# Performance work log

Measured on AMD Instinct MI355X. Metric: run time of the kernel, lower is better.

Reference implementation:

```python
import jax, jax.numpy as jnp
import numpy as np

N_NODES = 100000
N_EDGES = 1600000
D_IN = 64


def _graph_conv(x, edge_src, edge_dst, W, b, n_nodes):
    # gather source features along edges, mean-aggregate at destinations,
    # then linear transform + ReLU (standard GraphConv semantics)
    msgs = x[edge_src]  # [E, d]
    agg = jax.ops.segment_sum(msgs, edge_dst, num_segments=n_nodes)  # [N, d]
    deg = jax.ops.segment_sum(jnp.ones((edge_src.shape[0],), x.dtype), edge_dst,
                              num_segments=n_nodes)  # [N]
    agg = agg / jnp.maximum(deg, 1.0)[:, None]
    return jax.nn.relu(agg @ W + b)


def setup_inputs() -> dict:
    key = jax.random.key(0)
    ks = jax.random.split(key, 6)
    node_features = jax.random.normal(ks[0], (N_NODES, D_IN), dtype=jnp.float32)
    edge_src = jax.random.randint(ks[1], (N_EDGES,), 0, N_NODES)
    edge_dst = jax.random.randint(ks[2], (N_EDGES,), 0, N_NODES)
    W1 = jax.random.normal(ks[3], (D_IN, 64), dtype=jnp.float32) * (1.0 / np.sqrt(D_IN))
    b1 = jnp.zeros((64,), jnp.float32)
    W2 = jax.random.normal(ks[4], (64, 32), dtype=jnp.float32) * (1.0 / np.sqrt(64))
    b2 = jnp.zeros((32,), jnp.float32)
    Wd = jax.random.normal(ks[5], (1, 1), dtype=jnp.float32)
    bd = jnp.zeros((1,), jnp.float32)
    return {"node_features": node_features, "edge_src": edge_src, "edge_dst": edge_dst,
            "W1": W1, "b1": b1, "W2": W2, "b2": b2, "Wd": Wd, "bd": bd}


def reference(node_features, edge_src, edge_dst, W1, b1, W2, b2, Wd, bd):
    n_nodes = node_features.shape[0]
    x = _graph_conv(node_features, edge_src, edge_dst, W1, b1, n_nodes)  # [N, 64]
    x = _graph_conv(x, edge_src, edge_dst, W2, b2, n_nodes)              # [N, 32]
    x = jnp.mean(x, axis=1, keepdims=True)                               # [N, 1]
    return jax.nn.sigmoid(x @ Wd + bd)                                   # [N, 1]
```

## Files before the change

kernel.cpp:

```cpp
#include <hip/hip_runtime.h>
#include <hip/hip_bf16.h>

#define N_NODES 100000
#define N_EDGES 1600000
#define N_PAD   100096
#define BSHIFT  10
#define NBUCKET 98
#define BCAP    19456
#define EPB     4096
#define NSCAT   391
#define NGEMM1  1563
#define PCAP    34816
#define ZROW    N_NODES

__device__ __forceinline__ unsigned short f32_to_bf16(float f) {
    unsigned int u = __float_as_uint(f);
    unsigned int r = (u + 0x7fffu + ((u >> 16) & 1u)) >> 16;
    return (unsigned short)r;
}
__device__ __forceinline__ float bf16_lo(unsigned int p) {
    return __uint_as_float(p << 16);
}
__device__ __forceinline__ float bf16_hi(unsigned int p) {
    return __uint_as_float(p & 0xffff0000u);
}

__global__ void __launch_bounds__(256) k1_scatter_gemm64(
    const int* __restrict__ src, const int* __restrict__ dst,
    int* __restrict__ bcur, unsigned int* __restrict__ tmp,
    const float4* __restrict__ X4, const float* __restrict__ W,
    unsigned short* __restrict__ Y, int n_edges, int M) {
    extern __shared__ char smem[];
    int t = threadIdx.x;
    if (blockIdx.x < NSCAT) {
        int* lh = (int*)smem;
        int e0 = blockIdx.x * EPB;
        int e1 = min(e0 + EPB, n_edges);
        if (t < 128) lh[t] = 0;
        __syncthreads();
        int ls[16], ld[16];
        #pragma unroll
        for (int j = 0; j < 16; j++) {
            int e = e0 + t + j * 256;
            if (e < e1) {
                ls[j] = src[e];
                ld[j] = dst[e];
                atomicAdd(&lh[ld[j] >> BSHIFT], 1);
            }
        }
        __syncthreads();
        if (t < NBUCKET) {
            int c = lh[t];
            lh[t] = (c > 0) ? atomicAdd(&bcur[t], c) : 0;
        }
        __syncthreads();
        #pragma unroll
        for (int j = 0; j < 16; j++) {
            int e = e0 + t + j * 256;
            if (e < e1) {
                int b = ld[j] >> BSHIFT;
                int p = atomicAdd(&lh[b], 1);
                if (p < BCAP)
                    tmp[(size_t)b * BCAP + p] =
                        ((unsigned)ls[j] << BSHIFT) | (unsigned)(ld[j] & 1023);
            }
        }
        return;
    }
    float* sx = (float*)smem;
    float* sw = sx + 64 * 65;
    int base = (blockIdx.x - NSCAT) * 64;
    for (int i = t; i < 64 * 16; i += 256) {
        int r = i >> 4, c4 = i & 15;
        int row = base + r;
        float4 v = make_float4(0.f, 0.f, 0.f, 0.f);
        if (row < M) v = X4[(size_t)row * 16 + c4];
        sx[r * 65 + c4 * 4 + 0] = v.x; sx[r * 65 + c4 * 4 + 1] = v.y;
        sx[r * 65 + c4 * 4 + 2] = v.z; sx[r * 65 + c4 * 4 + 3] = v.w;
    }
    float4* sw4 = (float4*)sw;
    const float4* W4 = (const float4*)W;
    for (int i = t; i < 64 * 16; i += 256) sw4[i] = W4[i];
    __syncthreads();

    int tm = t & 15;
    int tn = t >> 4;
    float acc[4][4] = {{0.f}};
    #pragma unroll 8
    for (int k = 0; k < 64; k++) {
        float4 b = sw4[k * 16 + tn];
        float a0 = sx[(tm * 4 + 0) * 65 + k], a1 = sx[(tm * 4 + 1) * 65 + k];
        float a2 = sx[(tm * 4 + 2) * 65 + k], a3 = sx[(tm * 4 + 3) * 65 + k];
        acc[0][0] = fmaf(a0, b.x, acc[0][0]); acc[0][1] = fmaf(a0, b.y, acc[0][1]);
        acc[0][2] = fmaf(a0, b.z, acc[0][2]); acc[0][3] = fmaf(a0, b.w, acc[0][3]);
        acc[1][0] = fmaf(a1, b.x, acc[1][0]); acc[1][1] = fmaf(a1, b.y, acc[1][1]);
        acc[1][2] = fmaf(a1, b.z, acc[1][2]); acc[1][3] = fmaf(a1, b.w, acc[1][3]);
        acc[2][0] = fmaf(a2, b.x, acc[2][0]); acc[2][1] = fmaf(a2, b.y, acc[2][1]);
        acc[2][2] = fmaf(a2, b.z, acc[2][2]); acc[2][3] = fmaf(a2, b.w, acc[2][3]);
        acc[3][0] = fmaf(a3, b.x, acc[3][0]); acc[3][1] = fmaf(a3, b.y, acc[3][1]);
        acc[3][2] = fmaf(a3, b.z, acc[3][2]); acc[3][3] = fmaf(a3, b.w, acc[3][3]);
    }
    #pragma unroll
    for (int i = 0; i < 4; i++) {
        int row = base + tm * 4 + i;
        if (row <= M) {
            ushort4 p;
            p.x = f32_to_bf16(acc[i][0]); p.y = f32_to_bf16(acc[i][1]);
            p.z = f32_to_bf16(acc[i][2]); p.w = f32_to_bf16(acc[i][3]);
            *(ushort4*)&Y[(size_t)row * 64 + tn * 4] = p;
        }
    }
}

__global__ void __launch_bounds__(1024) bucket_to_csr(
    const unsigned int* __restrict__ tmp, const int* __restrict__ bcur,
    int2* __restrict__ meta, int* __restrict__ col, int n_nodes) {
    __shared__ int nh[1024];
    __shared__ int npref[1024];
    int b = blockIdx.x;
    int t = threadIdx.x;
    int m = min(bcur[b], BCAP);
    int cbase = b * PCAP;
    nh[t] = 0;
    __syncthreads();
    const unsigned int* te = tmp + (size_t)b * BCAP;
    for (int i = t; i < m; i += 1024) atomicAdd(&nh[te[i] & 1023], 1);
    __syncthreads();
    int d  = nh[t];
    int pc = (d + 31) & ~31;
    npref[t] = pc;
    __syncthreads();
    for (int off = 1; off < 1024; off <<= 1) {
        int u = (t >= off) ? npref[t - off] : 0;
        __syncthreads();
        npref[t] += u;
        __syncthreads();
    }
    int begin = cbase + npref[t] - pc;
    int node = (b << BSHIFT) + t;
    if (node < n_nodes) meta[node] = make_int2(begin, d);
    for (int j = d; j < pc; j++) col[begin + j] = ZROW;
    nh[t] = begin;
    __syncthreads();
    for (int i = t; i < m; i += 1024) {
        unsigned int e = te[i];
        int pos = atomicAdd(&nh[e & 1023], 1);
        col[pos] = (int)(e >> BSHIFT);
    }
}

__global__ void __launch_bounds__(256) gemm_n32(const float4* __restrict__ X4,
                                                const float* __restrict__ W,
                                                unsigned short* __restrict__ Z, int M) {
    __shared__ float sx[128][65];
    __shared__ float sw[64 * 32];
    int t = threadIdx.x;
    int base = blockIdx.x * 128;
    for (int i = t; i < 128 * 16; i += 256) {
        int r = i >> 4, c4 = i & 15;
        int row = base + r;
        float4 v = make_float4(0.f, 0.f, 0.f, 0.f);
        if (row < M) v = X4[(size_t)row * 16 + c4];
        sx[r][c4 * 4 + 0] = v.x; sx[r][c4 * 4 + 1] = v.y;
        sx[r][c4 * 4 + 2] = v.z; sx[r][c4 * 4 + 3] = v.w;
    }
    float4* sw4 = (float4*)sw;
    const float4* W4 = (const float4*)W;
    for (int i = t; i < 64 * 8; i += 256) sw4[i] = W4[i];
    __syncthreads();

    int tm = t & 31;
    int tn = t >> 5;
    float acc[4][4] = {{0.f}};
    #pragma unroll 8
    for (int k = 0; k < 64; k++) {
        float4 b = sw4[k * 8 + tn];
        float a0 = sx[tm * 4 + 0][k], a1 = sx[tm * 4 + 1][k];
        float a2 = sx[tm * 4 + 2][k], a3 = sx[tm * 4 + 3][k];
        acc[0][0] = fmaf(a0, b.x, acc[0][0]); acc[0][1] = fmaf(a0, b.y, acc[0][1]);
        acc[0][2] = fmaf(a0, b.z, acc[0][2]); acc[0][3] = fmaf(a0, b.w, acc[0][3]);
        acc[1][0] = fmaf(a1, b.x, acc[1][0]); acc[1][1] = fmaf(a1, b.y, acc[1][1]);
        acc[1][2] = fmaf(a1, b.z, acc[1][2]); acc[1][3] = fmaf(a1, b.w, acc[1][3]);
        acc[2][0] = fmaf(a2, b.x, acc[2][0]); acc[2][1] = fmaf(a2, b.y, acc[2][1]);
        acc[2][2] = fmaf(a2, b.z, acc[2][2]); acc[2][3] = fmaf(a2, b.w, acc[2][3]);
        acc[3][0] = fmaf(a3, b.x, acc[3][0]); acc[3][1] = fmaf(a3, b.y, acc[3][1]);
        acc[3][2] = fmaf(a3, b.z, acc[3][2]); acc[3][3] = fmaf(a3, b.w, acc[3][3]);
    }
    #pragma unroll
    for (int i = 0; i < 4; i++) {
        int row = base + tm * 4 + i;
        if (row <= M) {
            ushort4 p;
            p.x = f32_to_bf16(acc[i][0]); p.y = f32_to_bf16(acc[i][1]);
            p.z = f32_to_bf16(acc[i][2]); p.w = f32_to_bf16(acc[i][3]);
            *(ushort4*)&Z[(size_t)row * 32 + tn * 4] = p;
        }
    }
}

__global__ void __launch_bounds__(256) gather_relu64(
    const uint4* __restrict__ Y4, const int2* __restrict__ meta,
    const int* __restrict__ col, const float* __restrict__ b1,
    float4* __restrict__ H4, int n_nodes) {
    int n = blockIdx.x * 4 + (threadIdx.x >> 6);
    if (n >= n_nodes) return;
    int lane = threadIdx.x & 63;
    int g = lane >> 3;
    int c = lane & 7;
    int2 md = meta[n];
    int beg = md.x;
    int d = md.y;

    float acc[8] = {0.f, 0.f, 0.f, 0.f, 0.f, 0.f, 0.f, 0.f};
    for (int i = 0; i < d; i += 32) {
        int s0 = col[beg + i + g];
        int s1 = col[beg + i + g + 8];
        int s2 = col[beg + i + g + 16];
        int s3 = col[beg + i + g + 24];
        uint4 v0 = Y4[(size_t)s0 * 8 + c];
        uint4 v1 = Y4[(size_t)s1 * 8 + c];
        uint4 v2 = Y4[(size_t)s2 * 8 + c];
        uint4 v3 = Y4[(size_t)s3 * 8 + c];
        acc[0] += (bf16_lo(v0.x) + bf16_lo(v1.x)) + (bf16_lo(v2.x) + bf16_lo(v3.x));
        acc[1] += (bf16_hi(v0.x) + bf16_hi(v1.x)) + (bf16_hi(v2.x) + bf16_hi(v3.x));
        acc[2] += (bf16_lo(v0.y) + bf16_lo(v1.y)) + (bf16_lo(v2.y) + bf16_lo(v3.y));
        acc[3] += (bf16_hi(v0.y) + bf16_hi(v1.y)) + (bf16_hi(v2.y) + bf16_hi(v3.y));
        acc[4] += (bf16_lo(v0.z) + bf16_lo(v1.z)) + (bf16_lo(v2.z) + bf16_lo(v3.z));
        acc[5] += (bf16_hi(v0.z) + bf16_hi(v1.z)) + (bf16_hi(v2.z) + bf16_hi(v3.z));
        acc[6] += (bf16_lo(v0.w) + bf16_lo(v1.w)) + (bf16_lo(v2.w) + bf16_lo(v3.w));
        acc[7] += (bf16_hi(v0.w) + bf16_hi(v1.w)) + (bf16_hi(v2.w) + bf16_hi(v3.w));
    }
    #pragma unroll
    for (int m = 8; m <= 32; m <<= 1) {
        #pragma unroll
        for (int q = 0; q < 8; q++) acc[q] += __shfl_xor(acc[q], m);
    }
    float inv = 1.0f / fmaxf((float)d, 1.0f);
    const float4* b1_4 = (const float4*)b1;
    float4 ba = b1_4[c * 2], bb = b1_4[c * 2 + 1];
    if (g == 0) {
        float4 o0, o1;
        o0.x = fmaxf(fmaf(acc[0], inv, ba.x), 0.f);
        o0.y = fmaxf(fmaf(acc[1], inv, ba.y), 0.f);
        o0.z = fmaxf(fmaf(acc[2], inv, ba.z), 0.f);
        o0.w = fmaxf(fmaf(acc[3], inv, ba.w), 0.f);
        o1.x = fmaxf(fmaf(acc[4], inv, bb.x), 0.f);
        o1.y = fmaxf(fmaf(acc[5], inv, bb.y), 0.f);
        o1.z = fmaxf(fmaf(acc[6], inv, bb.z), 0.f);
        o1.w = fmaxf(fmaf(acc[7], inv, bb.w), 0.f);
        H4[(size_t)n * 16 + c * 2]     = o0;
        H4[(size_t)n * 16 + c * 2 + 1] = o1;
    }
}

__global__ void __launch_bounds__(256) gather_final32(
    const uint4* __restrict__ Z4, const int2* __restrict__ meta,
    const int* __restrict__ col, const float* __restrict__ b2,
    const float* __restrict__ Wd, const float* __restrict__ bd,
    float* __restrict__ out, int n_nodes) {
    int n = blockIdx.x * 4 + (threadIdx.x >> 6);
    if (n >= n_nodes) return;
    int lane = threadIdx.x & 63;
    int g = lane >> 2;
    int c = lane & 3;
    int2 md = meta[n];
    int beg = md.x;
    int d = md.y;

    float acc[8] = {0.f, 0.f, 0.f, 0.f, 0.f, 0.f, 0.f, 0.f};
    for (int i = 0; i < d; i += 32) {
        int s0 = col[beg + i + g];
        int s1 = col[beg + i + g + 16];
        uint4 v0 = Z4[(size_t)s0 * 4 + c];
        uint4 v1 = Z4[(size_t)s1 * 4 + c];
        acc[0] += bf16_lo(v0.x) + bf16_lo(v1.x);
        acc[1] += bf16_hi(v0.x) + bf16_hi(v1.x);
        acc[2] += bf16_lo(v0.y) + bf16_lo(v1.y);
        acc[3] += bf16_hi(v0.y) + bf16_hi(v1.y);
        acc[4] += bf16_lo(v0.z) + bf16_lo(v1.z);
        acc[5] += bf16_hi(v0.z) + bf16_hi(v1.z);
        acc[6] += bf16_lo(v0.w) + bf16_lo(v1.w);
        acc[7] += bf16_hi(v0.w) + bf16_hi(v1.w);
    }
    #pragma unroll
    for (int m = 4; m <= 32; m <<= 1) {
        #pragma unroll
        for (int q = 0; q < 8; q++) acc[q] += __shfl_xor(acc[q], m);
    }
    float inv = 1.0f / fmaxf((float)d, 1.0f);
    const float4* b2_4 = (const float4*)b2;
    float4 ba = b2_4[c * 2], bb = b2_4[c * 2 + 1];
    float local = 0.f;
    local += fmaxf(fmaf(acc[0], inv, ba.x), 0.f);
    local += fmaxf(fmaf(acc[1], inv, ba.y), 0.f);
    local += fmaxf(fmaf(acc[2], inv, ba.z), 0.f);
    local += fmaxf(fmaf(acc[3], inv, ba.w), 0.f);
    local += fmaxf(fmaf(acc[4], inv, bb.x), 0.f);
    local += fmaxf(fmaf(acc[5], inv, bb.y), 0.f);
    local += fmaxf(fmaf(acc[6], inv, bb.z), 0.f);
    local += fmaxf(fmaf(acc[7], inv, bb.w), 0.f);
    local += __shfl_xor(local, 1);
    local += __shfl_xor(local, 2);
    if (lane == 0) {
        float z = fmaf(local * (1.0f / 32.0f), Wd[0], bd[0]);
        out[n] = 1.0f / (1.0f + __expf(-z));
    }
}

extern "C" void kernel_launch(void* const* d_in, const int* in_sizes, int n_in,
                              void* d_out, int out_size, void* d_ws, size_t ws_size,
                              hipStream_t stream) {
    const float* x    = (const float*)d_in[0];
    const int*   esrc = (const int*)d_in[1];
    const int*   edst = (const int*)d_in[2];
    const float* W1   = (const float*)d_in[3];
    const float* b1   = (const float*)d_in[4];
    const float* W2   = (const float*)d_in[5];
    const float* b2   = (const float*)d_in[6];
    const float* Wd   = (const float*)d_in[7];
    const float* bd   = (const float*)d_in[8];
    float* out = (float*)d_out;

    int*  bcur = (int*)d_ws;
    int2* meta = (int2*)(bcur + 128);
    int*  col  = (int*)(meta + N_PAD);
    float* h   = (float*)(col + (size_t)NBUCKET * PCAP + 1024);
    unsigned int* tmp = (unsigned int*)h;
    unsigned short* y  = (unsigned short*)(h + (size_t)N_NODES * 64);
    unsigned short* z2 = y + (size_t)(N_NODES + 1) * 64;

    hipMemsetAsync((void*)bcur, 0, 128 * sizeof(int), stream);

    k1_scatter_gemm64<<<NSCAT + NGEMM1, 256, 33024, stream>>>(
        esrc, edst, bcur, tmp, (const float4*)x, W1, y, N_EDGES, N_NODES);
    bucket_to_csr<<<NBUCKET, 1024, 0, stream>>>(tmp, bcur, meta, col, N_NODES);
    gather_relu64<<<(N_NODES + 3) / 4, 256, 0, stream>>>(
        (const uint4*)y, meta, col, b1, (float4*)h, N_NODES);
    gemm_n32<<<(N_NODES + 127) / 128, 256, 0, stream>>>((const float4*)h, W2, z2, N_NODES);
    gather_final32<<<(N_NODES + 3) / 4, 256, 0, stream>>>(
        (const uint4*)z2, meta, col, b2, Wd, bd, out, N_NODES);
}
```

Baseline: 237.5 us.

## Fuse second-layer GEMM into first gather epilogue, widen final gather parallelism

The separate gemm_n32 kernel is removed. Each wave now multiplies its aggregated, ReLU'd 64-wide node row by W2 held in registers, reduces across lanes with shuffles and writes the bf16 result directly, so the fp32 intermediate h is never written to or read back from global memory. The final gather is remapped to 8 edge groups by 8 lanes with uint2 loads and four edges per iteration, to keep more loads in flight. The changes add register pressure from the W2 fragments and extra shuffle reductions per node.

Measured after the change: 296.6 us. +24.9%, slower.

```diff
diff --git a/kernel.cpp b/kernel.cpp
--- a/kernel.cpp
+++ b/kernel.cpp
@@ -149,64 +149,30 @@
     }
 }
 
-__global__ void __launch_bounds__(256) gemm_n32(const float4* __restrict__ X4,
-                                                const float* __restrict__ W,
-                                                unsigned short* __restrict__ Z, int M) {
-    __shared__ float sx[128][65];
-    __shared__ float sw[64 * 32];
-    int t = threadIdx.x;
-    int base = blockIdx.x * 128;
-    for (int i = t; i < 128 * 16; i += 256) {
-        int r = i >> 4, c4 = i & 15;
-        int row = base + r;
-        float4 v = make_float4(0.f, 0.f, 0.f, 0.f);
-        if (row < M) v = X4[(size_t)row * 16 + c4];
-        sx[r][c4 * 4 + 0] = v.x; sx[r][c4 * 4 + 1] = v.y;
-        sx[r][c4 * 4 + 2] = v.z; sx[r][c4 * 4 + 3] = v.w;
-    }
-    float4* sw4 = (float4*)sw;
-    const float4* W4 = (const float4*)W;
-    for (int i = t; i < 64 * 8; i += 256) sw4[i] = W4[i];
-    __syncthreads();
-
-    int tm = t & 31;
-    int tn = t >> 5;
-    float acc[4][4] = {{0.f}};
-    #pragma unroll 8
-    for (int k = 0; k < 64; k++) {
-        float4 b = sw4[k * 8 + tn];
-        float a0 = sx[tm * 4 + 0][k], a1 = sx[tm * 4 + 1][k];
-        float a2 = sx[tm * 4 + 2][k], a3 = sx[tm * 4 + 3][k];
-        acc[0][0] = fmaf(a0, b.x, acc[0][0]); acc[0][1] = fmaf(a0, b.y, acc[0][1]);
-        acc[0][2] = fmaf(a0, b.z, acc[0][2]); acc[0][3] = fmaf(a0, b.w, acc[0][3]);
-        acc[1][0] = fmaf(a1, b.x, acc[1][0]); acc[1][1] = fmaf(a1, b.y, acc[1][1]);
-        acc[1][2] = fmaf(a1, b.z, acc[1][2]); acc[1][3] = fmaf(a1, b.w, acc[1][3]);
-        acc[2][0] = fmaf(a2, b.x, acc[2][0]); acc[2][1] = fmaf(a2, b.y, acc[2][1]);
-        acc[2][2] = fmaf(a2, b.z, acc[2][2]); acc[2][3] = fmaf(a2, b.w, acc[2][3]);
-        acc[3][0] = fmaf(a3, b.x, acc[3][0]); acc[3][1] = fmaf(a3, b.y, acc[3][1]);
-        acc[3][2] = fmaf(a3, b.z, acc[3][2]); acc[3][3] = fmaf(a3, b.w, acc[3][3]);
-    }
-    #pragma unroll
-    for (int i = 0; i < 4; i++) {
-        int row = base + tm * 4 + i;
-        if (row <= M) {
-            ushort4 p;
-            p.x = f32_to_bf16(acc[i][0]); p.y = f32_to_bf16(acc[i][1]);
-            p.z = f32_to_bf16(acc[i][2]); p.w = f32_to_bf16(acc[i][3]);
-            *(ushort4*)&Z[(size_t)row * 32 + tn * 4] = p;
-        }
-    }
-}
-
-__global__ void __launch_bounds__(256) gather_relu64(
+__global__ void __launch_bounds__(256) gather1_fused(
     const uint4* __restrict__ Y4, const int2* __restrict__ meta,
     const int* __restrict__ col, const float* __restrict__ b1,
-    float4* __restrict__ H4, int n_nodes) {
-    int n = blockIdx.x * 4 + (threadIdx.x >> 6);
-    if (n >= n_nodes) return;
+    const float* __restrict__ W2, unsigned short* __restrict__ Z,
+    int n_nodes) {
     int lane = threadIdx.x & 63;
     int g = lane >> 3;
     int c = lane & 7;
+    const float4* b1_4 = (const float4*)b1;
+    float4 ba = b1_4[c * 2], bb = b1_4[c * 2 + 1];
+    const float4* W2_4 = (const float4*)W2;
+    float4 wr[8];
+    #pragma unroll
+    for (int q = 0; q < 8; q++) wr[q] = W2_4[(8 * c + q) * 8 + g];
+
+    int n = blockIdx.x * 4 + (threadIdx.x >> 6);
+    if (n > n_nodes) return;
+    if (n == n_nodes) {
+        if (c == 0) {
+            ushort4 p = make_ushort4(0, 0, 0, 0);
+            *(ushort4*)&Z[(size_t)n * 32 + 4 * g] = p;
+        }
+        return;
+    }
     int2 md = meta[n];
     int beg = md.x;
     int d = md.y;
@@ -236,71 +202,84 @@
         for (int q = 0; q < 8; q++) acc[q] += __shfl_xor(acc[q], m);
     }
     float inv = 1.0f / fmaxf((float)d, 1.0f);
-    const float4* b1_4 = (const float4*)b1;
-    float4 ba = b1_4[c * 2], bb = b1_4[c * 2 + 1];
-    if (g == 0) {
-        float4 o0, o1;
-        o0.x = fmaxf(fmaf(acc[0], inv, ba.x), 0.f);
-        o0.y = fmaxf(fmaf(acc[1], inv, ba.y), 0.f);
-        o0.z = fmaxf(fmaf(acc[2], inv, ba.z), 0.f);
-        o0.w = fmaxf(fmaf(acc[3], inv, ba.w), 0.f);
-        o1.x = fmaxf(fmaf(acc[4], inv, bb.x), 0.f);
-        o1.y = fmaxf(fmaf(acc[5], inv, bb.y), 0.f);
-        o1.z = fmaxf(fmaf(acc[6], inv, bb.z), 0.f);
-        o1.w = fmaxf(fmaf(acc[7], inv, bb.w), 0.f);
-        H4[(size_t)n * 16 + c * 2]     = o0;
-        H4[(size_t)n * 16 + c * 2 + 1] = o1;
+    float hv[8];
+    hv[0] = fmaxf(fmaf(acc[0], inv, ba.x), 0.f);
+    hv[1] = fmaxf(fmaf(acc[1], inv, ba.y), 0.f);
+    hv[2] = fmaxf(fmaf(acc[2], inv, ba.z), 0.f);
+    hv[3] = fmaxf(fmaf(acc[3], inv, ba.w), 0.f);
+    hv[4] = fmaxf(fmaf(acc[4], inv, bb.x), 0.f);
+    hv[5] = fmaxf(fmaf(acc[5], inv, bb.y), 0.f);
+    hv[6] = fmaxf(fmaf(acc[6], inv, bb.z), 0.f);
+    hv[7] = fmaxf(fmaf(acc[7], inv, bb.w), 0.f);
+    float z0 = 0.f, z1 = 0.f, z2 = 0.f, z3 = 0.f;
+    #pragma unroll
+    for (int q = 0; q < 8; q++) {
+        z0 = fmaf(hv[q], wr[q].x, z0);
+        z1 = fmaf(hv[q], wr[q].y, z1);
+        z2 = fmaf(hv[q], wr[q].z, z2);
+        z3 = fmaf(hv[q], wr[q].w, z3);
+    }
+    #pragma unroll
+    for (int m = 1; m <= 4; m <<= 1) {
+        z0 += __shfl_xor(z0, m);
+        z1 += __shfl_xor(z1, m);
+        z2 += __shfl_xor(z2, m);
+        z3 += __shfl_xor(z3, m);
+    }
+    if (c == 0) {
+        ushort4 p;
+        p.x = f32_to_bf16(z0); p.y = f32_to_bf16(z1);
+        p.z = f32_to_bf16(z2); p.w = f32_to_bf16(z3);
+        *(ushort4*)&Z[(size_t)n * 32 + 4 * g] = p;
     }
 }
 
 __global__ void __launch_bounds__(256) gather_final32(
-    const uint4* __restrict__ Z4, const int2* __restrict__ meta,
+    const uint2* __restrict__ Z2, const int2* __restrict__ meta,
     const int* __restrict__ col, const float* __restrict__ b2,
     const float* __restrict__ Wd, const float* __restrict__ bd,
     float* __restrict__ out, int n_nodes) {
     int n = blockIdx.x * 4 + (threadIdx.x >> 6);
     if (n >= n_nodes) return;
     int lane = threadIdx.x & 63;
-    int g = lane >> 2;
-    int c = lane & 3;
+    int g = lane >> 3;
+    int c = lane & 7;
     int2 md = meta[n];
     int beg = md.x;
     int d = md.y;
 
-    float acc[8] = {0.f, 0.f, 0.f, 0.f, 0.f, 0.f, 0.f, 0.f};
+    float a0 = 0.f, a1 = 0.f, a2 = 0.f, a3 = 0.f;
     for (int i = 0; i < d; i += 32) {
         int s0 = col[beg + i + g];
-        int s1 = col[beg + i + g + 16];
-        uint4 v0 = Z4[(size_t)s0 * 4 + c];
-        uint4 v1 = Z4[(size_t)s1 * 4 + c];
-        acc[0] += bf16_lo(v0.x) + bf16_lo(v1.x);
-        acc[1] += bf16_hi(v0.x) + bf16_hi(v1.x);
-        acc[2] += bf16_lo(v0.y) + bf16_lo(v1.y);
-        acc[3] += bf16_hi(v0.y) + bf16_hi(v1.y);
-        acc[4] += bf16_lo(v0.z) + bf16_lo(v1.z);
-        acc[5] += bf16_hi(v0.z) + bf16_hi(v1.z);
-        acc[6] += bf16_lo(v0.w) + bf16_lo(v1.w);
-        acc[7] += bf16_hi(v0.w) + bf16_hi(v1.w);
-    }
-    #pragma unroll
-    for (int m = 4; m <= 32; m <<= 1) {
-        #pragma unroll
-        for (int q = 0; q < 8; q++) acc[q] += __shfl_xor(acc[q], m);
+        int s1 = col[beg + i + g + 8];
+        int s2 = col[beg + i + g + 16];
+        int s3 = col[beg + i + g + 24];
+        uint2 v0 = Z2[(size_t)s0 * 8 + c];
+        uint2 v1 = Z2[(size_t)s1 * 8 + c];
+        uint2 v2 = Z2[(size_t)s2 * 8 + c];
+        uint2 v3 = Z2[(size_t)s3 * 8 + c];
+        a0 += (bf16_lo(v0.x) + bf16_lo(v1.x)) + (bf16_lo(v2.x) + bf16_lo(v3.x));
+        a1 += (bf16_hi(v0.x) + bf16_hi(v1.x)) + (bf16_hi(v2.x) + bf16_hi(v3.x));
+        a2 += (bf16_lo(v0.y) + bf16_lo(v1.y)) + (bf16_lo(v2.y) + bf16_lo(v3.y));
+        a3 += (bf16_hi(v0.y) + bf16_hi(v1.y)) + (bf16_hi(v2.y) + bf16_hi(v3.y));
+    }
+    #pragma unroll
+    for (int m = 8; m <= 32; m <<= 1) {
+        a0 += __shfl_xor(a0, m);
+        a1 += __shfl_xor(a1, m);
+        a2 += __shfl_xor(a2, m);
+        a3 += __shfl_xor(a3, m);
     }
     float inv = 1.0f / fmaxf((float)d, 1.0f);
     const float4* b2_4 = (const float4*)b2;
-    float4 ba = b2_4[c * 2], bb = b2_4[c * 2 + 1];
-    float local = 0.f;
-    local += fmaxf(fmaf(acc[0], inv, ba.x), 0.f);
-    local += fmaxf(fmaf(acc[1], inv, ba.y), 0.f);
-    local += fmaxf(fmaf(acc[2], inv, ba.z), 0.f);
-    local += fmaxf(fmaf(acc[3], inv, ba.w), 0.f);
-    local += fmaxf(fmaf(acc[4], inv, bb.x), 0.f);
-    local += fmaxf(fmaf(acc[5], inv, bb.y), 0.f);
-    local += fmaxf(fmaf(acc[6], inv, bb.z), 0.f);
-    local += fmaxf(fmaf(acc[7], inv, bb.w), 0.f);
+    float4 ba = b2_4[c];
+    float local = fmaxf(fmaf(a0, inv, ba.x), 0.f)
+                + fmaxf(fmaf(a1, inv, ba.y), 0.f)
+                + fmaxf(fmaf(a2, inv, ba.z), 0.f)
+                + fmaxf(fmaf(a3, inv, ba.w), 0.f);
     local += __shfl_xor(local, 1);
     local += __shfl_xor(local, 2);
+    local += __shfl_xor(local, 4);
     if (lane == 0) {
         float z = fmaf(local * (1.0f / 32.0f), Wd[0], bd[0]);
         out[n] = 1.0f / (1.0f + __expf(-z));
@@ -324,9 +303,8 @@
     int*  bcur = (int*)d_ws;
     int2* meta = (int2*)(bcur + 128);
     int*  col  = (int*)(meta + N_PAD);
-    float* h   = (float*)(col + (size_t)NBUCKET * PCAP + 1024);
-    unsigned int* tmp = (unsigned int*)h;
-    unsigned short* y  = (unsigned short*)(h + (size_t)N_NODES * 64);
+    unsigned int* tmp = (unsigned int*)(col + (size_t)NBUCKET * PCAP + 1024);
+    unsigned short* y  = (unsigned short*)(tmp + (size_t)NBUCKET * BCAP);
     unsigned short* z2 = y + (size_t)(N_NODES + 1) * 64;
 
     hipMemsetAsync((void*)bcur, 0, 128 * sizeof(int), stream);
@@ -334,9 +312,8 @@
     k1_scatter_gemm64<<<NSCAT + NGEMM1, 256, 33024, stream>>>(
         esrc, edst, bcur, tmp, (const float4*)x, W1, y, N_EDGES, N_NODES);
     bucket_to_csr<<<NBUCKET, 1024, 0, stream>>>(tmp, bcur, meta, col, N_NODES);
-    gather_relu64<<<(N_NODES + 3) / 4, 256, 0, stream>>>(
-        (const uint4*)y, meta, col, b1, (float4*)h, N_NODES);
-    gemm_n32<<<(N_NODES + 127) / 128, 256, 0, stream>>>((const float4*)h, W2, z2, N_NODES);
+    gather1_fused<<<(N_NODES + 1 + 3) / 4, 256, 0, stream>>>(
+        (const uint4*)y, meta, col, b1, W2, z2, N_NODES);
     gather_final32<<<(N_NODES + 3) / 4, 256, 0, stream>>>(
-        (const uint4*)z2, meta, col, b2, Wd, bd, out, N_NODES);
-}
+        (const uint2*)z2, meta, col, b2, Wd, bd, out, N_NODES);
+}
```
